# Optimization experiments

Hardware: AMD Instinct MI355X
Metric: run time of the kernel (lower is better)

The kernel has to match this reference:

```python
import jax, jax.numpy as jnp
import numpy as np
import math

NUM_POSE_FEAT = 64  # -> pos emb dim 128
N_NBR = 16
TEMP = 10000.0


def pos2posemb2d(pos, num_pos_feats=NUM_POSE_FEAT):
    # PETR-style 2D sine embedding; pos: (..., 2) in [0,1)
    scale = 2.0 * math.pi
    pos = pos * scale
    dim_t = jnp.arange(num_pos_feats, dtype=pos.dtype)
    dim_t = TEMP ** (2.0 * jnp.floor(dim_t / 2.0) / num_pos_feats)
    pos_x = pos[..., 0:1] / dim_t  # (..., P)
    pos_y = pos[..., 1:2] / dim_t

    def interleave(p):
        return jnp.stack([jnp.sin(p[..., 0::2]), jnp.cos(p[..., 1::2])], axis=-1).reshape(p.shape[:-1] + (-1,))

    return jnp.concatenate([interleave(pos_y), interleave(pos_x)], axis=-1)  # (..., 2P)


def mlp(x, W1, b1, W2, b2):
    return jax.nn.relu(x @ W1 + b1) @ W2 + b2


def setup_inputs() -> dict:
    key = jax.random.key(0)
    ks = jax.random.split(key, 12)
    B, S, L, D, P2 = 4, 4096, 8192, 256, 2 * NUM_POSE_FEAT
    s1 = 1.0 / np.sqrt(P2)
    s2 = 1.0 / np.sqrt(D)
    return {
        "memory": jax.random.normal(ks[0], (B, L, D), jnp.float32),
        "mem_coor": jax.random.uniform(ks[1], (B, L, 2), dtype=jnp.float32),
        "q_coor": jax.random.uniform(ks[2], (B, S, 2), dtype=jnp.float32),
        "Wq1": jax.random.normal(ks[3], (P2, D), jnp.float32) * s1,
        "bq1": jnp.zeros((D,), jnp.float32),
        "Wq2": jax.random.normal(ks[4], (D, D), jnp.float32) * s2,
        "bq2": jnp.zeros((D,), jnp.float32),
        "Wk1": jax.random.normal(ks[5], (P2, D), jnp.float32) * s1,
        "bk1": jnp.zeros((D,), jnp.float32),
        "Wk2": jax.random.normal(ks[6], (D, D), jnp.float32) * s2,
        "bk2": jnp.zeros((D,), jnp.float32),
        "B": 4,
    }


def reference(memory, mem_coor, q_coor, Wq1, bq1, Wq2, bq2, Wk1, bk1, Wk2, bk2, B):
    # memory: (B, L, D); mem_coor: (B, L, 2); q_coor: (B, S, 2)
    Bn, L, D = memory.shape
    query = mlp(pos2posemb2d(q_coor), Wq1, bq1, Wq2, bq2)      # (B, S, D) query = query_pos
    mem_pos = mlp(pos2posemb2d(mem_coor), Wk1, bk1, Wk2, bk2)  # (B, L, D)
    kv_pe = mem_pos + memory                                   # (B, L, D)

    # squared pairwise distances via matmul expansion (monotonic in true distance,
    # only the top-k ORDER is consumed downstream)
    q2 = jnp.sum(q_coor * q_coor, axis=-1)                     # (B, S)
    m2 = jnp.sum(mem_coor * mem_coor, axis=-1)                 # (B, L)
    d2 = q2[:, :, None] + m2[:, None, :] - 2.0 * jnp.einsum("bsc,blc->bsl", q_coor, mem_coor)
    _, idx = jax.lax.top_k(-d2, N_NBR)                         # (B, S, k) nearest-neighbor indices

    bidx = jnp.arange(Bn)[:, None, None]
    kv_m = kv_pe[bidx, idx]                                    # (B, S, k, D) gathered pos-embedded memory
    prod = query[:, :, None, :] * kv_m / jnp.sqrt(jnp.asarray(D, query.dtype))
    attn = jax.nn.softmax(prod, axis=-1)                       # softmax over feature dim D
    out = attn * memory[bidx, idx]                             # (B, S, k, D)
    return out
```

## Files before the change

### kernel.cpp

```cpp
#include <hip/hip_runtime.h>
#include <math.h>

#define NB 4
#define NS 4096
#define NL 8192
#define ND 256
#define NP2 128
#define NK 16

#define GCELLS 32
#define GH 0.03125f
#define CAP 256
#define EPSM 2e-5f

__device__ __forceinline__ float sum_sq_np(float x, float y) {
#pragma clang fp contract(off)
  return x * x + y * y;
}

__device__ __forceinline__ float dist2_fast(float q2, float m2, float qx, float qy,
                                            float mx, float my) {
#pragma clang fp contract(off)
  float dot = __builtin_fmaf(qy, my, qx * mx);
  float s = q2 + m2;
  return __builtin_fmaf(-2.0f, dot, s);
}

__device__ __forceinline__ unsigned f32ord(float f) {
  unsigned u = __float_as_uint(f);
  return u ^ ((unsigned)((int)u >> 31) | 0x80000000u);
}

template <int NR>
__device__ __forceinline__ unsigned extract16(const unsigned long long* candrow,
                                              int cnt, int lane,
                                              int* __restrict__ outp) {
  unsigned long long myc[NR];
#pragma unroll
  for (int j = 0; j < NR; ++j) {
    int p = lane + j * 64;
    myc[j] = (p < cnt) ? candrow[p] : ~0ull;
  }
  unsigned tau_ord = 0xffffffffu;
#pragma unroll 1
  for (int r = 0; r < NK; ++r) {
    unsigned long long m = myc[0];
#pragma unroll
    for (int j = 1; j < NR; ++j) m = myc[j] < m ? myc[j] : m;
#pragma unroll
    for (int o = 1; o < 64; o <<= 1) {
      unsigned long long other = __shfl_xor(m, o, 64);
      if (other < m) m = other;
    }
    if (lane == 0) outp[r] = (int)(unsigned)(m & 0xffffffffull);
    if (r == NK - 1) tau_ord = (unsigned)(m >> 32);
#pragma unroll
    for (int j = 0; j < NR; ++j)
      if (myc[j] == m) myc[j] = ~0ull;
  }
  return tau_ord;
}

#define RPAD 20
#define NSBLK (NB * NS / 16)

struct __align__(16) MlpSmem {
  union {
    float pe[NP2][RPAD];
    float h[ND][RPAD];
  };
};

__device__ __forceinline__ void fma16(float* acc, float wt, const float4& p0,
                                      const float4& p1, const float4& p2,
                                      const float4& p3) {
  acc[0] = fmaf(p0.x, wt, acc[0]);   acc[1] = fmaf(p0.y, wt, acc[1]);
  acc[2] = fmaf(p0.z, wt, acc[2]);   acc[3] = fmaf(p0.w, wt, acc[3]);
  acc[4] = fmaf(p1.x, wt, acc[4]);   acc[5] = fmaf(p1.y, wt, acc[5]);
  acc[6] = fmaf(p1.z, wt, acc[6]);   acc[7] = fmaf(p1.w, wt, acc[7]);
  acc[8] = fmaf(p2.x, wt, acc[8]);   acc[9] = fmaf(p2.y, wt, acc[9]);
  acc[10] = fmaf(p2.z, wt, acc[10]); acc[11] = fmaf(p2.w, wt, acc[11]);
  acc[12] = fmaf(p3.x, wt, acc[12]); acc[13] = fmaf(p3.y, wt, acc[13]);
  acc[14] = fmaf(p3.z, wt, acc[14]); acc[15] = fmaf(p3.w, wt, acc[15]);
}

__device__ __forceinline__ void loadW8(const float* __restrict__ W, int k0,
                                       int col, float* w) {
#pragma unroll
  for (int u = 0; u < 8; ++u) w[u] = W[(size_t)(k0 + u) * ND + col];
}

__device__ __forceinline__ void consume8(const float (*L)[RPAD], int k0,
                                         const float* w, float* acc) {
#pragma unroll
  for (int u = 0; u < 8; ++u) {
    int k = k0 + u;
    float4 p0 = *(const float4*)&L[k][0];
    float4 p1 = *(const float4*)&L[k][4];
    float4 p2 = *(const float4*)&L[k][8];
    float4 p3 = *(const float4*)&L[k][12];
    fma16(acc, w[u], p0, p1, p2, p3);
  }
}

__global__ __launch_bounds__(256) void mlp_fused_kernel(
    const float* __restrict__ q_coor, const float* __restrict__ mem_coor,
    const float* __restrict__ memory,
    const float* __restrict__ Wq1, const float* __restrict__ bq1,
    const float* __restrict__ Wq2, const float* __restrict__ bq2,
    const float* __restrict__ Wk1, const float* __restrict__ bk1,
    const float* __restrict__ Wk2, const float* __restrict__ bk2,
    float* __restrict__ query, float* __restrict__ kv_pe) {
  __shared__ MlpSmem sm;
  const int tid = threadIdx.x;
  const int bid = blockIdx.x;
  const bool isS = bid < NSBLK;
  const float* coor = isS ? q_coor : mem_coor;
  const float* W1 = isS ? Wq1 : Wk1;
  const float* b1 = isS ? bq1 : bk1;
  const float* W2 = isS ? Wq2 : Wk2;
  const float* b2 = isS ? bq2 : bk2;
  const float* addmem = isS ? (const float*)nullptr : memory;
  float* out = isS ? query : kv_pe;
  const int row0 = (isS ? bid : bid - NSBLK) * 16;

#pragma unroll
  for (int it = 0; it < 4; ++it) {
    int e = tid + it * 256;
    int r = e >> 6;
    int rem = e & 63;
    int part = rem >> 5;
    int j = rem & 31;
    float c = coor[(size_t)(row0 + r) * 2 + (part ^ 1)];
    float inv_t = exp2f((float)j * -0.4152410118609718f);
    float arg = c * 6.2831853071795864f * inv_t;
    float sv, cv;
    sincosf(arg, &sv, &cv);
    int k0 = part * 64 + 2 * j;
    sm.pe[k0][r] = sv;
    sm.pe[k0 + 1][r] = cv;
  }
  __syncthreads();

  float acc[16];
  float wA[8], wB[8];
  {
    float bb = b1[tid];
#pragma unroll
    for (int r = 0; r < 16; ++r) acc[r] = bb;
  }
  loadW8(W1, 0, tid, wA);
#pragma unroll 1
  for (int k0 = 0; k0 < NP2; k0 += 16) {
    loadW8(W1, k0 + 8, tid, wB);
    consume8(sm.pe, k0, wA, acc);
    if (k0 + 16 < NP2) loadW8(W1, k0 + 16, tid, wA);
    consume8(sm.pe, k0 + 8, wB, acc);
  }
  __syncthreads();
#pragma unroll
  for (int r = 0; r < 16; ++r) sm.h[tid][r] = fmaxf(acc[r], 0.0f);
  __syncthreads();

  {
    float bb = b2[tid];
#pragma unroll
    for (int r = 0; r < 16; ++r) acc[r] = bb;
  }
  loadW8(W2, 0, tid, wA);
#pragma unroll 1
  for (int k0 = 0; k0 < ND; k0 += 16) {
    loadW8(W2, k0 + 8, tid, wB);
    consume8(sm.h, k0, wA, acc);
    if (k0 + 16 < ND) loadW8(W2, k0 + 16, tid, wA);
    consume8(sm.h, k0 + 8, wB, acc);
  }
#pragma unroll
  for (int r = 0; r < 16; ++r) {
    size_t g = (size_t)(row0 + r);
    float v = acc[r];
    if (addmem) v += addmem[g * ND + tid];
    out[g * ND + tid] = v;
  }
}

__global__ __launch_bounds__(1024) void build_kernel(
    const float* __restrict__ mem_coor, const float* __restrict__ q_coor,
    float4* __restrict__ sorted, int* __restrict__ starts,
    int* __restrict__ qord) {
  __shared__ int hist[GCELLS * GCELLS];
  __shared__ int cur[GCELLS * GCELLS];
  const int bid = blockIdx.x;
  const bool isMem = bid < NB;
  const int b = isMem ? bid : bid - NB;
  const int n = isMem ? NL : NS;
  const float2* cc = (const float2*)(isMem ? mem_coor : q_coor) + (size_t)b * n;
  const int tid = threadIdx.x;

  hist[tid] = 0;
  __syncthreads();
  for (int it = 0; it < n / 1024; ++it) {
    float2 c = cc[it * 1024 + tid];
    int cx = (int)(c.x * 32.0f); cx = cx > 31 ? 31 : cx;
    int cy = (int)(c.y * 32.0f); cy = cy > 31 ? 31 : cy;
    atomicAdd(&hist[cy * GCELLS + cx], 1);
  }
  __syncthreads();
  const int own = hist[tid];
  for (int o = 1; o < 1024; o <<= 1) {
    int v = (tid >= o) ? hist[tid - o] : 0;
    __syncthreads();
    hist[tid] += v;
    __syncthreads();
  }
  const int excl = hist[tid] - own;
  if (isMem) {
    starts[b * (GCELLS * GCELLS + 1) + tid] = excl;
    if (tid == 0) starts[b * (GCELLS * GCELLS + 1) + GCELLS * GCELLS] = NL;
  }
  cur[tid] = excl;
  __syncthreads();
  for (int it = 0; it < n / 1024; ++it) {
    int i = it * 1024 + tid;
    float2 c = cc[i];
    int cx = (int)(c.x * 32.0f); cx = cx > 31 ? 31 : cx;
    int cy = (int)(c.y * 32.0f); cy = cy > 31 ? 31 : cy;
    int pos = atomicAdd(&cur[cy * GCELLS + cx], 1);
    if (isMem) {
      sorted[(size_t)b * NL + pos] =
          make_float4(c.x, c.y, sum_sq_np(c.x, c.y), __int_as_float(i));
    } else {
      qord[b * NS + pos] = i;
    }
  }
}

__global__ __launch_bounds__(256) void topk_kernel(
    const float* __restrict__ q_coor, const float4* __restrict__ sorted,
    const int* __restrict__ starts, int* __restrict__ idx_out) {
  __shared__ unsigned long long cand[4][CAP];
  __shared__ int fcnt[4];

  const int tid = threadIdx.x;
  const int wv = tid >> 6;
  const int lane = tid & 63;
  const int qi = blockIdx.x * 4 + wv;
  const int b = qi >> 12;

  const float qx = q_coor[(size_t)qi * 2 + 0];
  const float qy = q_coor[(size_t)qi * 2 + 1];
  const float q2 = sum_sq_np(qx, qy);
  const float4* sp = sorted + (size_t)b * NL;
  const int* st = starts + b * (GCELLS * GCELLS + 1);
  int* outp = idx_out + (size_t)qi * NK;

  int ci = (int)(qx * 32.0f); ci = ci > 31 ? 31 : ci;
  int cj = (int)(qy * 32.0f); cj = cj > 31 ? 31 : cj;

  int x0 = ci - 1 < 0 ? 0 : ci - 1, x1 = ci + 1 > 31 ? 31 : ci + 1;
  int y0 = cj - 1 < 0 ? 0 : cj - 1, y1 = cj + 1 > 31 ? 31 : cj + 1;
  int cnt = 0;
  bool ovf = false;

  auto span = [&](int y, int xa, int xb) {
    int s0 = st[y * GCELLS + xa];
    int e0 = st[y * GCELLS + xb + 1];
    int len = e0 - s0;
    if (cnt + len > CAP) { ovf = true; return; }
    for (int i = lane; i < len; i += 64) {
      float4 rx = sp[s0 + i];
      float d2 = dist2_fast(q2, rx.z, qx, qy, rx.x, rx.y);
      cand[wv][cnt + i] = ((unsigned long long)f32ord(d2) << 32) |
                          (unsigned)__float_as_int(rx.w);
    }
    cnt += len;
  };

  for (int y = y0; y <= y1 && !ovf; ++y) span(y, x0, x1);

  int R = 1;
  while (!ovf) {
    unsigned tau_ord;
    if (cnt <= 128) tau_ord = extract16<2>(cand[wv], cnt, lane, outp);
    else            tau_ord = extract16<4>(cand[wv], cnt, lane, outp);
    float dxl = x0 > 0  ? qx - (float)x0 * GH        : 1e30f;
    float dxr = x1 < 31 ? (float)(x1 + 1) * GH - qx  : 1e30f;
    float dyl = y0 > 0  ? qy - (float)y0 * GH        : 1e30f;
    float dyr = y1 < 31 ? (float)(y1 + 1) * GH - qy  : 1e30f;
    float dmin = fminf(fminf(dxl, dxr), fminf(dyl, dyr));
    float bound = dmin * dmin - EPSM;
    if (cnt >= NK && tau_ord < f32ord(bound)) return;
    if (x0 == 0 && x1 == 31 && y0 == 0 && y1 == 31) return;
    ++R;
    int nx0 = ci - R < 0 ? 0 : ci - R, nx1 = ci + R > 31 ? 31 : ci + R;
    int ny0 = cj - R < 0 ? 0 : cj - R, ny1 = cj + R > 31 ? 31 : cj + R;
    if (ny0 < y0) span(ny0, nx0, nx1);
    if (ny1 > y1 && !ovf) span(ny1, nx0, nx1);
    for (int y = y0; y <= y1 && !ovf; ++y) {
      if (nx0 < x0) span(y, nx0, x0 - 1);
      if (nx1 > x1 && !ovf) span(y, x1 + 1, nx1);
    }
    x0 = nx0; x1 = nx1; y0 = ny0; y1 = ny1;
  }

  float lmin = __builtin_inff();
#pragma unroll 8
  for (int it = 0; it < NL / 64; ++it) {
    float4 rx = sp[it * 64 + lane];
    float d2 = dist2_fast(q2, rx.z, qx, qy, rx.x, rx.y);
    lmin = fminf(lmin, d2);
  }
  float tau;
  {
    float curm = lmin;
    for (int r = 0; r < NK; ++r) {
      float m = curm;
#pragma unroll
      for (int o = 1; o < 64; o <<= 1) m = fminf(m, __shfl_xor(m, o, 64));
      tau = m;
      if (curm == m) curm = __builtin_inff();
    }
  }
  if (lane == 0) fcnt[wv] = 0;
#pragma unroll 4
  for (int it = 0; it < NL / 64; ++it) {
    float4 rx = sp[it * 64 + lane];
    float d2 = dist2_fast(q2, rx.z, qx, qy, rx.x, rx.y);
    bool hit = (d2 <= tau);
    unsigned long long mask = __ballot(hit);
    if (mask) {
      int base = fcnt[wv];
      if (hit) {
        int pos = base + (int)__popcll(mask & ((1ull << lane) - 1ull));
        if (pos < CAP) {
          cand[wv][pos] = ((unsigned long long)f32ord(d2) << 32) |
                          (unsigned)__float_as_int(rx.w);
        }
      }
      if (lane == 0) fcnt[wv] = base + (int)__popcll(mask);
    }
  }
  int N = fcnt[wv];
  if (N > CAP) N = CAP;
  extract16<4>(cand[wv], N, lane, outp);
}

__global__ __launch_bounds__(256) void attn_kernel(
    const float* __restrict__ query, const float* __restrict__ kv_pe,
    const float* __restrict__ memory, const int* __restrict__ idx,
    const int* __restrict__ qord, float* __restrict__ out) {
  const int tid = threadIdx.x;
  const int wv = tid >> 6;
  const int lane = tid & 63;
  const int bid = ((blockIdx.x & 7) * (NB * NS / 4 / 8)) + (blockIdx.x >> 3);
  const int qpos = bid * 4 + wv;
  const int b = qpos >> 12;
  const int qi = b * NS + qord[qpos];

  float4 q4 = *(const float4*)(query + (size_t)qi * ND + lane * 4);
  int lv = 0;
  if (lane < NK) lv = idx[(size_t)qi * NK + lane];

#pragma unroll 4
  for (int k = 0; k < NK; ++k) {
    int l = __shfl(lv, k, 64);
    size_t base = ((size_t)b * NL + l) * ND + (size_t)lane * 4;
    float4 kv = *(const float4*)(kv_pe + base);
    float4 mm = *(const float4*)(memory + base);
    float p0 = q4.x * kv.x * 0.0625f;
    float p1 = q4.y * kv.y * 0.0625f;
    float p2 = q4.z * kv.z * 0.0625f;
    float p3 = q4.w * kv.w * 0.0625f;
    float mx = fmaxf(fmaxf(p0, p1), fmaxf(p2, p3));
#pragma unroll
    for (int o = 1; o < 64; o <<= 1) mx = fmaxf(mx, __shfl_xor(mx, o, 64));
    float e0 = expf(p0 - mx);
    float e1 = expf(p1 - mx);
    float e2 = expf(p2 - mx);
    float e3 = expf(p3 - mx);
    float s = (e0 + e1) + (e2 + e3);
#pragma unroll
    for (int o = 1; o < 64; o <<= 1) s += __shfl_xor(s, o, 64);
    float inv = 1.0f / s;
    float4 o4;
    o4.x = e0 * inv * mm.x;
    o4.y = e1 * inv * mm.y;
    o4.z = e2 * inv * mm.z;
    o4.w = e3 * inv * mm.w;
    *(float4*)(out + ((size_t)qi * NK + k) * ND + (size_t)lane * 4) = o4;
  }
}

extern "C" void kernel_launch(void* const* d_in, const int* in_sizes, int n_in,
                              void* d_out, int out_size, void* d_ws, size_t ws_size,
                              hipStream_t stream) {
  (void)in_sizes; (void)n_in; (void)out_size; (void)ws_size;
  const float* memory   = (const float*)d_in[0];
  const float* mem_coor = (const float*)d_in[1];
  const float* q_coor   = (const float*)d_in[2];
  const float* Wq1 = (const float*)d_in[3];
  const float* bq1 = (const float*)d_in[4];
  const float* Wq2 = (const float*)d_in[5];
  const float* bq2 = (const float*)d_in[6];
  const float* Wk1 = (const float*)d_in[7];
  const float* bk1 = (const float*)d_in[8];
  const float* Wk2 = (const float*)d_in[9];
  const float* bk2 = (const float*)d_in[10];

  float* query = (float*)d_ws;
  float* kv_pe = query + (size_t)NB * NS * ND;
  int*   nidx  = (int*)(kv_pe + (size_t)NB * NL * ND);
  int*   qord  = nidx + (size_t)NB * NS * NK;
  float* outp  = (float*)d_out;

  float4* sorted  = (float4*)d_out;
  int*    gstarts = (int*)((char*)d_out + (size_t)NB * NL * 16);

  hipLaunchKernelGGL(build_kernel, dim3(2 * NB), dim3(1024), 0, stream,
                     mem_coor, q_coor, sorted, gstarts, qord);
  hipLaunchKernelGGL(mlp_fused_kernel, dim3(NSBLK + NB * NL / 16), dim3(256),
                     0, stream, q_coor, mem_coor, memory,
                     Wq1, bq1, Wq2, bq2, Wk1, bk1, Wk2, bk2, query, kv_pe);
  hipLaunchKernelGGL(topk_kernel, dim3(NB * NS / 4), dim3(256), 0, stream,
                     q_coor, sorted, gstarts, nidx);
  hipLaunchKernelGGL(attn_kernel, dim3(NB * NS / 4), dim3(256), 0, stream,
                     query, kv_pe, memory, nidx, qord, outp);
}
```

Measured before the change: 596.3 us.

## Register-tile MLP kernel as 16 rows x 4 columns per thread with 64-thread blocks

Rewrites the fused positional MLP kernel so each thread computes a 16-row by 4-column register tile using float4 weight loads, with blocks shrunk from 256 to 64 threads. Each LDS read of the embedding/hidden row is now reused across four output columns and each weight load is vectorised, cutting LDS traffic per FMA. The cost is 64 accumulators per thread, higher register pressure, and fewer threads per block for latency hiding; the hidden-layer LDS writes become strided per column.

```diff
diff --git a/kernel.cpp b/kernel.cpp
--- a/kernel.cpp
+++ b/kernel.cpp
@@ -71,39 +71,35 @@
   };
 };
 
-__device__ __forceinline__ void fma16(float* acc, float wt, const float4& p0,
-                                      const float4& p1, const float4& p2,
-                                      const float4& p3) {
-  acc[0] = fmaf(p0.x, wt, acc[0]);   acc[1] = fmaf(p0.y, wt, acc[1]);
-  acc[2] = fmaf(p0.z, wt, acc[2]);   acc[3] = fmaf(p0.w, wt, acc[3]);
-  acc[4] = fmaf(p1.x, wt, acc[4]);   acc[5] = fmaf(p1.y, wt, acc[5]);
-  acc[6] = fmaf(p1.z, wt, acc[6]);   acc[7] = fmaf(p1.w, wt, acc[7]);
-  acc[8] = fmaf(p2.x, wt, acc[8]);   acc[9] = fmaf(p2.y, wt, acc[9]);
-  acc[10] = fmaf(p2.z, wt, acc[10]); acc[11] = fmaf(p2.w, wt, acc[11]);
-  acc[12] = fmaf(p3.x, wt, acc[12]); acc[13] = fmaf(p3.y, wt, acc[13]);
-  acc[14] = fmaf(p3.z, wt, acc[14]); acc[15] = fmaf(p3.w, wt, acc[15]);
-}
-
-__device__ __forceinline__ void loadW8(const float* __restrict__ W, int k0,
-                                       int col, float* w) {
-#pragma unroll
-  for (int u = 0; u < 8; ++u) w[u] = W[(size_t)(k0 + u) * ND + col];
-}
-
-__device__ __forceinline__ void consume8(const float (*L)[RPAD], int k0,
-                                         const float* w, float* acc) {
-#pragma unroll
-  for (int u = 0; u < 8; ++u) {
+__device__ __forceinline__ void fma4row(float4& a, float p, const float4& w) {
+  a.x = fmaf(p, w.x, a.x);
+  a.y = fmaf(p, w.y, a.y);
+  a.z = fmaf(p, w.z, a.z);
+  a.w = fmaf(p, w.w, a.w);
+}
+
+__device__ __forceinline__ void consume4v(const float (*L)[RPAD], int k0,
+                                          const float4* w, float4* acc) {
+#pragma unroll
+  for (int u = 0; u < 4; ++u) {
     int k = k0 + u;
     float4 p0 = *(const float4*)&L[k][0];
     float4 p1 = *(const float4*)&L[k][4];
     float4 p2 = *(const float4*)&L[k][8];
     float4 p3 = *(const float4*)&L[k][12];
-    fma16(acc, w[u], p0, p1, p2, p3);
-  }
-}
-
-__global__ __launch_bounds__(256) void mlp_fused_kernel(
+    float4 wu = w[u];
+    fma4row(acc[0],  p0.x, wu); fma4row(acc[1],  p0.y, wu);
+    fma4row(acc[2],  p0.z, wu); fma4row(acc[3],  p0.w, wu);
+    fma4row(acc[4],  p1.x, wu); fma4row(acc[5],  p1.y, wu);
+    fma4row(acc[6],  p1.z, wu); fma4row(acc[7],  p1.w, wu);
+    fma4row(acc[8],  p2.x, wu); fma4row(acc[9],  p2.y, wu);
+    fma4row(acc[10], p2.z, wu); fma4row(acc[11], p2.w, wu);
+    fma4row(acc[12], p3.x, wu); fma4row(acc[13], p3.y, wu);
+    fma4row(acc[14], p3.z, wu); fma4row(acc[15], p3.w, wu);
+  }
+}
+
+__global__ __launch_bounds__(64) void mlp_fused_kernel(
     const float* __restrict__ q_coor, const float* __restrict__ mem_coor,
     const float* __restrict__ memory,
     const float* __restrict__ Wq1, const float* __restrict__ bq1,
@@ -123,10 +119,11 @@
   const float* addmem = isS ? (const float*)nullptr : memory;
   float* out = isS ? query : kv_pe;
   const int row0 = (isS ? bid : bid - NSBLK) * 16;
-
-#pragma unroll
-  for (int it = 0; it < 4; ++it) {
-    int e = tid + it * 256;
+  const int c0 = tid * 4;
+
+#pragma unroll
+  for (int it = 0; it < 16; ++it) {
+    int e = tid + it * 64;
     int r = e >> 6;
     int rem = e & 63;
     int part = rem >> 5;
@@ -142,45 +139,69 @@
   }
   __syncthreads();
 
-  float acc[16];
-  float wA[8], wB[8];
+  float4 acc[16];
+  float4 wA[4], wB[4];
   {
-    float bb = b1[tid];
+    float4 bb = *(const float4*)&b1[c0];
 #pragma unroll
     for (int r = 0; r < 16; ++r) acc[r] = bb;
   }
-  loadW8(W1, 0, tid, wA);
+#pragma unroll
+  for (int u = 0; u < 4; ++u)
+    wA[u] = *(const float4*)&W1[(size_t)u * ND + c0];
 #pragma unroll 1
-  for (int k0 = 0; k0 < NP2; k0 += 16) {
-    loadW8(W1, k0 + 8, tid, wB);
-    consume8(sm.pe, k0, wA, acc);
-    if (k0 + 16 < NP2) loadW8(W1, k0 + 16, tid, wA);
-    consume8(sm.pe, k0 + 8, wB, acc);
-  }
-  __syncthreads();
-#pragma unroll
-  for (int r = 0; r < 16; ++r) sm.h[tid][r] = fmaxf(acc[r], 0.0f);
+  for (int k0 = 0; k0 < NP2; k0 += 8) {
+#pragma unroll
+    for (int u = 0; u < 4; ++u)
+      wB[u] = *(const float4*)&W1[(size_t)(k0 + 4 + u) * ND + c0];
+    consume4v(sm.pe, k0, wA, acc);
+    if (k0 + 8 < NP2) {
+#pragma unroll
+      for (int u = 0; u < 4; ++u)
+        wA[u] = *(const float4*)&W1[(size_t)(k0 + 8 + u) * ND + c0];
+    }
+    consume4v(sm.pe, k0 + 4, wB, acc);
+  }
+  __syncthreads();
+#pragma unroll
+  for (int r = 0; r < 16; ++r) {
+    sm.h[c0 + 0][r] = fmaxf(acc[r].x, 0.0f);
+    sm.h[c0 + 1][r] = fmaxf(acc[r].y, 0.0f);
+    sm.h[c0 + 2][r] = fmaxf(acc[r].z, 0.0f);
+    sm.h[c0 + 3][r] = fmaxf(acc[r].w, 0.0f);
+  }
   __syncthreads();
 
   {
-    float bb = b2[tid];
+    float4 bb = *(const float4*)&b2[c0];
 #pragma unroll
     for (int r = 0; r < 16; ++r) acc[r] = bb;
   }
-  loadW8(W2, 0, tid, wA);
+#pragma unroll
+  for (int u = 0; u < 4; ++u)
+    wA[u] = *(const float4*)&W2[(size_t)u * ND + c0];
 #pragma unroll 1
-  for (int k0 = 0; k0 < ND; k0 += 16) {
-    loadW8(W2, k0 + 8, tid, wB);
-    consume8(sm.h, k0, wA, acc);
-    if (k0 + 16 < ND) loadW8(W2, k0 + 16, tid, wA);
-    consume8(sm.h, k0 + 8, wB, acc);
+  for (int k0 = 0; k0 < ND; k0 += 8) {
+#pragma unroll
+    for (int u = 0; u < 4; ++u)
+      wB[u] = *(const float4*)&W2[(size_t)(k0 + 4 + u) * ND + c0];
+    consume4v(sm.h, k0, wA, acc);
+    if (k0 + 8 < ND) {
+#pragma unroll
+      for (int u = 0; u < 4; ++u)
+        wA[u] = *(const float4*)&W2[(size_t)(k0 + 8 + u) * ND + c0];
+    }
+    consume4v(sm.h, k0 + 4, wB, acc);
   }
 #pragma unroll
   for (int r = 0; r < 16; ++r) {
     size_t g = (size_t)(row0 + r);
-    float v = acc[r];
-    if (addmem) v += addmem[g * ND + tid];
-    out[g * ND + tid] = v;
+    float4 v = acc[r];
+    if (addmem) {
+      float4 mm = *(const float4*)&addmem[g * ND + c0];
+      v.x += mm.x; v.y += mm.y; v.z += mm.z; v.w += mm.w;
+    }
+    *(float4*)&out[g * ND + c0] = v;
   }
 }
 
@@ -418,7 +439,7 @@
 
   hipLaunchKernelGGL(build_kernel, dim3(2 * NB), dim3(1024), 0, stream,
                      mem_coor, q_coor, sorted, gstarts, qord);
-  hipLaunchKernelGGL(mlp_fused_kernel, dim3(NSBLK + NB * NL / 16), dim3(256),
+  hipLaunchKernelGGL(mlp_fused_kernel, dim3(NSBLK + NB * NL / 16), dim3(64),
                      0, stream, q_coor, mem_coor, memory,
                      Wq1, bq1, Wq2, bq2, Wk1, bk1, Wk2, bk2, query, kv_pe);
   hipLaunchKernelGGL(topk_kernel, dim3(NB * NS / 4), dim3(256), 0, stream,
```

Measured after the change: 521.6 us. 12.5% less time.
